# Performance work log

Hardware: AMD Instinct MI355X
Metric: run time of the kernel (lower is better)

The kernel has to match this reference:

```python
import jax, jax.numpy as jnp
import numpy as np
from jax import lax

B, E, D, N, R, K = 4, 768, 1536, 16, 48, 4
H, W = 16, 16
L = H * W
NDIR = 4


def _perms():
    idx = np.arange(L)
    idx_v = np.arange(L).reshape(H, W).T.reshape(-1)  # column-major (vertical) scan order
    perms = [idx, idx[::-1].copy(), idx_v, idx_v[::-1].copy()]
    invs = [np.argsort(p) for p in perms]
    return [jnp.asarray(p) for p in perms], [jnp.asarray(p) for p in invs]

PERMS, INVS = _perms()


def setup_inputs() -> dict:
    key = jax.random.key(0)
    ks = jax.random.split(key, 10)
    hidden_states = jax.random.normal(ks[0], (B, L, E), jnp.float32)
    in_proj_w = jax.random.normal(ks[1], (2 * D, E), jnp.float32) * 0.02
    out_proj_w = jax.random.normal(ks[2], (E, D), jnp.float32) * 0.02
    conv_w = jax.random.normal(ks[3], (NDIR, D, K), jnp.float32) * 0.1
    conv_b = jax.random.normal(ks[4], (NDIR, D), jnp.float32) * 0.1
    xproj_w = jax.random.normal(ks[5], (NDIR, R + 2 * N, D), jnp.float32) * 0.02
    dt_init_std = R ** -0.5
    dtproj_w = jax.random.uniform(ks[6], (NDIR, D, R), jnp.float32, -dt_init_std, dt_init_std)
    dt = jnp.exp(jax.random.uniform(ks[7], (NDIR, D), jnp.float32)
                 * (np.log(0.1) - np.log(0.001)) + np.log(0.001))
    dt = jnp.clip(dt, 1e-4, None)
    dtproj_b = dt + jnp.log(-jnp.expm1(-dt))  # inverse-softplus init as in the module
    A_log = jnp.broadcast_to(
        jnp.log(jnp.arange(1, N + 1, dtype=jnp.float32))[None, None, :], (NDIR, D, N)).copy()
    D_param = jnp.ones((NDIR, D), jnp.float32)
    return dict(hidden_states=hidden_states, in_proj_w=in_proj_w, out_proj_w=out_proj_w,
                conv_w=conv_w, conv_b=conv_b, xproj_w=xproj_w, dtproj_w=dtproj_w,
                dtproj_b=dtproj_b, A_log=A_log, D_param=D_param)


def _mamba_dir(xz, cw, cb, xw, dtw, dtb, a_log, dpar):
    # xz: (B, 2D, L) in this direction's scan order
    x, z = xz[:, :D], xz[:, D:]
    # causal depthwise conv1d + SiLU (mamba_inner_fn conv path)
    x = lax.conv_general_dilated(x, cw[:, None, :], (1,), [(K - 1, 0)],
                                 feature_group_count=D,
                                 dimension_numbers=('NCH', 'OIH', 'NCH'))
    x = jax.nn.silu(x + cb[None, :, None])
    # x_proj -> dt, B, C
    x_dbl = jnp.einsum('bdl,kd->bkl', x, xw)
    dt, Bm, Cm = x_dbl[:, :R], x_dbl[:, R:R + N], x_dbl[:, R + N:]
    delta = jax.nn.softplus(jnp.einsum('brl,dr->bdl', dt, dtw) + dtb[None, :, None])
    A = -jnp.exp(a_log)                                  # (D, N)
    dA = jnp.exp(jnp.einsum('bdl,dn->lbdn', delta, A))   # (L, B, D, N)
    dBu = jnp.einsum('bdl,bnl,bdl->lbdn', delta, Bm, x)  # delta * B * u

    def step(h, inp):
        da, dbu = inp
        h = da * h + dbu
        return h, h

    h0 = jnp.zeros((x.shape[0], D, N), x.dtype)
    _, hs = lax.scan(step, h0, (dA, dBu))                # (L, B, D, N)
    y = jnp.einsum('lbdn,bnl->bdl', hs, Cm) + dpar[None, :, None] * x
    return y * jax.nn.silu(z)                            # gate, (B, D, L)


def reference(hidden_states, in_proj_w, out_proj_w, conv_w, conv_b,
              xproj_w, dtproj_w, dtproj_b, A_log, D_param):
    xz = jnp.einsum('ble,fe->bfl', hidden_states, in_proj_w)  # (B, 2D, L)
    out = jnp.zeros((hidden_states.shape[0], D, L), hidden_states.dtype)
    for i in range(NDIR):  # fixed small set of structurally distinct scan directions
        xz_i = xz[:, :, PERMS[i]]
        y = _mamba_dir(xz_i, conv_w[i], conv_b[i], xproj_w[i], dtproj_w[i],
                       dtproj_b[i], A_log[i], D_param[i])
        out = out + y[:, :, INVS[i]]  # multi_reverse then sum-fusion
    return jnp.einsum('bdl,ed->ble', out, out_proj_w)
```

## Files before the change

### kernel.cpp

```cpp
#include <hip/hip_runtime.h>
#include <hip/hip_bf16.h>

#define BI   4
#define LI   256
#define EI   768
#define DI   1536
#define NI   16
#define RI   48
#define KI   4
#define NDIRS 4
#define F2D  3072
#define MROWS 1024
#define LOG2E 1.4426950408889634f
#define LN2   0.6931471805599453f

typedef float    floatx2 __attribute__((ext_vector_type(2)));
typedef float    floatx4 __attribute__((ext_vector_type(4)));
typedef _Float16 halfx2  __attribute__((ext_vector_type(2)));
typedef _Float16 halfx4  __attribute__((ext_vector_type(4)));
typedef _Float16 halfx8  __attribute__((ext_vector_type(8)));

typedef __attribute__((address_space(3))) unsigned lds_u32;
typedef __attribute__((address_space(1))) const unsigned glb_u32;

__device__ __forceinline__ void load16(const _Float16* g, _Float16* l) {
    __builtin_amdgcn_global_load_lds((glb_u32*)g, (lds_u32*)l, 16, 0, 0);
}

__device__ __forceinline__ int perm_idx(int dir, int j) {
    switch (dir) {
        case 0:  return j;
        case 1:  return 255 - j;
        case 2:  return ((j & 15) << 4) | (j >> 4);
        default: return 255 - (((j & 15) << 4) | (j >> 4));
    }
}

template<int CTRL>
__device__ __forceinline__ float dpp_add(float p) {
    int t = __builtin_amdgcn_update_dpp(0, __builtin_bit_cast(int, p),
                                        CTRL, 0xf, 0xf, true);
    return p + __builtin_bit_cast(float, t);
}
__device__ __forceinline__ float grp8_sum(float p) {
    p = dpp_add<0xB1>(p);
    p = dpp_add<0x4E>(p);
    p = dpp_add<0x141>(p);
    return p;
}

template<int BM, int BN, int WGN, int FM, int FN>
__device__ __forceinline__ void gemm_core(const _Float16* __restrict__ Ah,
                                          const _Float16* __restrict__ Al, int lda,
                                          const _Float16* __restrict__ Bh,
                                          const _Float16* __restrict__ Bl, int ldb,
                                          int nChunks, _Float16* smem,
                                          floatx4 (&acc)[FM][FN]) {
    const int tid = threadIdx.x, lane = tid & 63, wave = tid >> 6;
    const int wave_m = wave / WGN, wave_n = wave % WGN;
    _Float16* sAh = smem;
    _Float16* sAl = smem + BM * 32;
    _Float16* sBh = smem + BM * 64;
    _Float16* sBl = smem + BM * 64 + BN * 32;
    const int rr = lane & 15, koff = (lane >> 4) * 8;
    const int arow = wave_m * FM * 16, brow = wave_n * FN * 16;

    for (int c = 0; c < nChunks; ++c) {
        for (int idx = tid; idx < BM * 4; idx += 256) {
            int r = idx >> 2, s = (idx & 3) * 8;
            load16(Ah + (size_t)r * lda + c * 32 + s, sAh + idx * 8);
            load16(Al + (size_t)r * lda + c * 32 + s, sAl + idx * 8);
        }
        for (int idx = tid; idx < BN * 4; idx += 256) {
            int r = idx >> 2, s = (idx & 3) * 8;
            load16(Bh + (size_t)r * ldb + c * 32 + s, sBh + idx * 8);
            load16(Bl + (size_t)r * ldb + c * 32 + s, sBl + idx * 8);
        }
        asm volatile("s_waitcnt vmcnt(0)" ::: "memory");
        __syncthreads();

        halfx8 ahf[FM], alf[FM], bhf[FN], blf[FN];
        #pragma unroll
        for (int i = 0; i < FM; ++i) {
            ahf[i] = *(const halfx8*)(sAh + (arow + i * 16 + rr) * 32 + koff);
            alf[i] = *(const halfx8*)(sAl + (arow + i * 16 + rr) * 32 + koff);
        }
        #pragma unroll
        for (int j = 0; j < FN; ++j) {
            bhf[j] = *(const halfx8*)(sBh + (brow + j * 16 + rr) * 32 + koff);
            blf[j] = *(const halfx8*)(sBl + (brow + j * 16 + rr) * 32 + koff);
        }
        #pragma unroll
        for (int i = 0; i < FM; ++i)
            #pragma unroll
            for (int j = 0; j < FN; ++j) {
                acc[i][j] = __builtin_amdgcn_mfma_f32_16x16x32_f16(ahf[i], bhf[j], acc[i][j], 0, 0, 0);
                acc[i][j] = __builtin_amdgcn_mfma_f32_16x16x32_f16(ahf[i], blf[j], acc[i][j], 0, 0, 0);
                acc[i][j] = __builtin_amdgcn_mfma_f32_16x16x32_f16(alf[i], bhf[j], acc[i][j], 0, 0, 0);
            }
        __syncthreads();
    }
}

__global__ __launch_bounds__(256) void k_splitall(
        const float* __restrict__ hs,  const float* __restrict__ wip,
        const float* __restrict__ wop, const float* __restrict__ xw,
        const float* __restrict__ dtw,
        _Float16* __restrict__ hsh,  _Float16* __restrict__ hsl,
        _Float16* __restrict__ wiph, _Float16* __restrict__ wipl,
        _Float16* __restrict__ woph, _Float16* __restrict__ wopl,
        _Float16* __restrict__ xwh,  _Float16* __restrict__ xwl,
        _Float16* __restrict__ dtwh, _Float16* __restrict__ dtwl) {
    int i4 = (blockIdx.x * 256 + threadIdx.x) * 4;
    floatx4 v;
    _Float16 *dh, *dl; int off;
    if (i4 < 786432)        { off = i4;           v = *(const floatx4*)(hs + off);  dh = hsh;  dl = hsl;  }
    else if (i4 < 3145728)  { off = i4 - 786432;  v = *(const floatx4*)(wip + off); dh = wiph; dl = wipl; }
    else if (i4 < 4325376)  { off = i4 - 3145728; v = *(const floatx4*)(wop + off); dh = woph; dl = wopl; }
    else if (i4 < 4816896)  { off = i4 - 4325376; v = *(const floatx4*)(xw + off);  dh = xwh;  dl = xwl;  }
    else {
        int t0 = i4 - 4816896;
        int col = t0 & 63, dr = t0 >> 6;
        floatx4 z = {0.f, 0.f, 0.f, 0.f};
        v = (col < 48) ? *(const floatx4*)(dtw + (size_t)dr * 48 + col) : z;
        dh = dtwh; dl = dtwl; off = t0;
    }
    halfx4 hh, hl;
    #pragma unroll
    for (int e = 0; e < 4; ++e) {
        _Float16 h = (_Float16)v[e];
        hh[e] = h; hl[e] = (_Float16)(v[e] - (float)h);
    }
    *(halfx4*)(dh + off) = hh;
    *(halfx4*)(dl + off) = hl;
}

__global__ __launch_bounds__(256) void k_inproj_t(const _Float16* __restrict__ Ah,
                                                  const _Float16* __restrict__ Al,
                                                  const _Float16* __restrict__ Bh,
                                                  const _Float16* __restrict__ Bl,
                                                  float* __restrict__ C) {
    __shared__ _Float16 smem[128 * 64 + 128 * 64];
    int row0 = blockIdx.x * 128, col0 = blockIdx.y * 128, k0 = blockIdx.z * 384;
    float* Cp = C + (size_t)blockIdx.z * MROWS * F2D;
    floatx4 acc[4][4] = {};
    gemm_core<128, 128, 2, 4, 4>(Ah + (size_t)row0 * EI + k0, Al + (size_t)row0 * EI + k0, EI,
                                 Bh + (size_t)col0 * EI + k0, Bl + (size_t)col0 * EI + k0, EI,
                                 12, smem, acc);
    int lane = threadIdx.x & 63, wave = threadIdx.x >> 6;
    int cc = lane & 15, q = lane >> 4;
    int rbase = row0 + (wave >> 1) * 64, cbase = col0 + (wave & 1) * 64;
    #pragma unroll
    for (int i = 0; i < 4; ++i)
        #pragma unroll
        for (int j = 0; j < 4; ++j)
            #pragma unroll
            for (int r = 0; r < 4; ++r)
                Cp[(size_t)(rbase + i * 16 + q * 4 + r) * F2D + cbase + j * 16 + cc] = acc[i][j][r];
}

__global__ __launch_bounds__(256) void k_outproj_t(const _Float16* __restrict__ Ah,
                                                   const _Float16* __restrict__ Al,
                                                   const _Float16* __restrict__ Bh,
                                                   const _Float16* __restrict__ Bl,
                                                   float* __restrict__ C) {
    __shared__ _Float16 smem[192 * 64];
    int row0 = blockIdx.x * 64, col0 = blockIdx.y * 128, k0 = blockIdx.z * 384;
    float* Cp = C + (size_t)blockIdx.z * MROWS * EI;
    floatx4 acc[2][4] = {};
    gemm_core<64, 128, 2, 2, 4>(Ah + (size_t)row0 * DI + k0, Al + (size_t)row0 * DI + k0, DI,
                                Bh + (size_t)col0 * DI + k0, Bl + (size_t)col0 * DI + k0, DI,
                                12, smem, acc);
    int lane = threadIdx.x & 63, wave = threadIdx.x >> 6;
    int cc = lane & 15, q = lane >> 4;
    int rbase = row0 + (wave >> 1) * 32, cbase = col0 + (wave & 1) * 64;
    #pragma unroll
    for (int i = 0; i < 2; ++i)
        #pragma unroll
        for (int j = 0; j < 4; ++j)
            #pragma unroll
            for (int r = 0; r < 4; ++r)
                Cp[(size_t)(rbase + i * 16 + q * 4 + r) * EI + cbase + j * 16 + cc] = acc[i][j][r];
}

__global__ __launch_bounds__(256) void k_osum(const float* __restrict__ oacc,
                                              float* __restrict__ out) {
    int i4 = (blockIdx.x * 256 + threadIdx.x) * 4;
    const size_t S = (size_t)MROWS * EI;
    floatx4 s = *(const floatx4*)(oacc + i4) + *(const floatx4*)(oacc + S + i4) +
                *(const floatx4*)(oacc + 2 * S + i4) + *(const floatx4*)(oacc + 3 * S + i4);
    *(floatx4*)(out + i4) = s;
}

__global__ __launch_bounds__(256) void k_xdbl_t(const _Float16* __restrict__ xh,
                                                const _Float16* __restrict__ xl,
                                                const _Float16* __restrict__ xwh,
                                                const _Float16* __restrict__ xwl,
                                                float* __restrict__ C) {
    __shared__ _Float16 smem[208 * 64];
    int row0 = blockIdx.x * 128, dir = blockIdx.y, k0 = blockIdx.z * 192;
    float* Cp = C + (size_t)blockIdx.z * NDIRS * MROWS * 80;
    floatx4 acc[2][5] = {};
    const size_t abase = ((size_t)dir * MROWS + row0) * DI + k0;
    const size_t bbase = (size_t)dir * 80 * DI + k0;
    gemm_core<128, 80, 1, 2, 5>(xh + abase, xl + abase, DI,
                                xwh + bbase, xwl + bbase, DI, 6, smem, acc);
    int lane = threadIdx.x & 63, wave = threadIdx.x >> 6;
    int cc = lane & 15, q = lane >> 4;
    int rbase = row0 + wave * 32;
    #pragma unroll
    for (int i = 0; i < 2; ++i)
        #pragma unroll
        for (int j = 0; j < 5; ++j)
            #pragma unroll
            for (int r = 0; r < 4; ++r)
                Cp[((size_t)dir * MROWS + rbase + i * 16 + q * 4 + r) * 80 + j * 16 + cc] = acc[i][j][r];
}

__global__ __launch_bounds__(256) void k_xsplit(const float* __restrict__ acc,
                                                _Float16* __restrict__ dtqh,
                                                _Float16* __restrict__ dtql,
                                                float* __restrict__ BCm) {
    const size_t PS = (size_t)NDIRS * MROWS * 80;
    int idx = blockIdx.x * 256 + threadIdx.x;
    int dir = idx / (MROWS * 96);
    int rem = idx - dir * MROWS * 96;
    int row = rem / 96, col = rem - row * 96;
    size_t rbase = (size_t)dir * MROWS + row;
    auto sum8 = [&](int c) {
        size_t o = rbase * 80 + c;
        float s = 0.f;
        #pragma unroll
        for (int kp = 0; kp < 8; ++kp) s += acc[kp * PS + o];
        return s;
    };
    if (col < 64) {
        float v = (col < 48) ? sum8(col) : 0.f;
        _Float16 h = (_Float16)v;
        dtqh[rbase * 64 + col] = h;
        dtql[rbase * 64 + col] = (_Float16)(v - (float)h);
    } else if (col < 80) {
        int n = col - 64;
        BCm[rbase * 32 + n * 2] = sum8(48 + n);
    } else {
        int n = col - 80;
        BCm[rbase * 32 + n * 2 + 1] = sum8(64 + n);
    }
}

__global__ __launch_bounds__(512) void k_conv4(const float* __restrict__ xz,
                                               const float* __restrict__ cw,
                                               const float* __restrict__ cb,
                                               _Float16* __restrict__ xh,
                                               _Float16* __restrict__ xl) {
    const size_t S = (size_t)MROWS * F2D;
    const int b = blockIdx.y, d0 = blockIdx.x * 16;
    const int tid = threadIdx.x;
    __shared__ float sx[256][18];

    for (int i = tid; i < 1024; i += 512) {
        int row = i >> 2, c4 = (i & 3) * 4;
        size_t o = ((size_t)b * 256 + row) * F2D + d0 + c4;
        floatx4 v = *(const floatx4*)(xz + o) + *(const floatx4*)(xz + S + o);
        floatx2 v0 = {v[0], v[1]}, v1 = {v[2], v[3]};
        *(floatx2*)&sx[row][c4]     = v0;
        *(floatx2*)&sx[row][c4 + 2] = v1;
    }
    __syncthreads();

    const int dsub = tid & 15, lg = tid >> 4;
    const int d = d0 + dsub, j0 = lg * 8;
    #pragma unroll
    for (int dir = 0; dir < NDIRS; ++dir) {
        floatx4 w = *(const floatx4*)(cw + ((size_t)dir * DI + d) * KI);
        float bias = cb[(size_t)dir * DI + d];
        float xm3 = (j0 >= 3) ? sx[perm_idx(dir, j0 - 3)][dsub] : 0.f;
        float xm2 = (j0 >= 2) ? sx[perm_idx(dir, j0 - 2)][dsub] : 0.f;
        float xm1 = (j0 >= 1) ? sx[perm_idx(dir, j0 - 1)][dsub] : 0.f;
        #pragma unroll
        for (int j = 0; j < 8; ++j) {
            float cur = sx[perm_idx(dir, j0 + j)][dsub];
            float s = bias + w[0] * xm3 + w[1] * xm2 + w[2] * xm1 + w[3] * cur;
            xm3 = xm2; xm2 = xm1; xm1 = cur;
            float x = s / (1.f + __expf(-s));
            _Float16 h = (_Float16)x;
            size_t o = ((size_t)dir * MROWS + b * 256 + j0 + j) * DI + d;
            xh[o] = h;
            xl[o] = (_Float16)(x - (float)h);
        }
    }
}

__global__ __launch_bounds__(256) void k_scan(const _Float16* __restrict__ dtqh,
                                              const _Float16* __restrict__ dtql,
                                              const _Float16* __restrict__ dtwh,
                                              const _Float16* __restrict__ dtwl,
                                              const float* __restrict__ dtb,
                                              const _Float16* __restrict__ xhg,
                                              const _Float16* __restrict__ xlg,
                                              const float* __restrict__ BCm,
                                              const float* __restrict__ A_log,
                                              const float* __restrict__ Dp,
                                              float* __restrict__ ydir) {
    const int dchunk = blockIdx.x, b = blockIdx.y, dir = blockIdx.z;
    const int tid = threadIdx.x, lane = tid & 63, wave = tid >> 6;
    const int dslot = tid >> 3;
    const int np = tid & 7;
    const int d0 = dchunk * 32, d = d0 + dslot;

    __shared__ float sdx[2][32][68];
    __shared__ float sbc[2][32][32];
    __shared__ float sY[2][32][32];

    const float Av0 = -__expf(A_log[((size_t)dir * DI + d) * NI + 2 * np]) * LOG2E;
    const float Av1 = -__expf(A_log[((size_t)dir * DI + d) * NI + 2 * np + 1]) * LOG2E;
    const float Dpar = Dp[(size_t)dir * DI + d];
    float h0 = 0.f, h1 = 0.f;

    const size_t dirrow = (size_t)dir * MROWS;
    const int srow = tid >> 3, sc4 = (tid & 7) * 4;

    const int rowhalf = wave >> 1, dhalf = wave & 1;
    const int rr = lane & 15, koff = (lane >> 4) * 8, q = lane >> 4;
    const size_t bfb = ((size_t)dir * DI + d0 + dhalf * 16 + rr) * 64;
    halfx8 bhf[2], blf[2];
    bhf[0] = *(const halfx8*)(dtwh + bfb + koff);
    bhf[1] = *(const halfx8*)(dtwh + bfb + 32 + koff);
    blf[0] = *(const halfx8*)(dtwl + bfb + koff);
    blf[1] = *(const halfx8*)(dtwl + bfb + 32 + koff);
    const float bias = dtb[(size_t)dir * DI + d0 + dhalf * 16 + rr];

    floatx4 rbc;
    halfx4 rxh, rxl;
    auto load_chunk = [&](int j0) {
        int row = b * 256 + j0 + srow;
        size_t o = (dirrow + row) * DI + d0 + sc4;
        rxh = *(const halfx4*)(xhg + o);
        rxl = *(const halfx4*)(xlg + o);
        rbc = *(const floatx4*)(BCm + (dirrow + row) * 32 + sc4);
    };
    halfx8 ahf[2], alf[2];
    auto load_afrag = [&](int c) {
        size_t o = (dirrow + b * 256 + c * 32 + rowhalf * 16 + rr) * 64;
        ahf[0] = *(const halfx8*)(dtqh + o + koff);
        ahf[1] = *(const halfx8*)(dtqh + o + 32 + koff);
        alf[0] = *(const halfx8*)(dtql + o + koff);
        alf[1] = *(const halfx8*)(dtql + o + 32 + koff);
    };
    auto stage = [&](int bf) {
        #pragma unroll
        for (int e = 0; e < 4; ++e)
            sdx[bf][sc4 + e][srow * 2 + 1] = (float)rxh[e] + (float)rxl[e];
        *(floatx4*)&sbc[bf][srow][sc4] = rbc;
    };
    auto mfma_delta = [&](int bf) {
        floatx4 acc = {};
        #pragma unroll
        for (int kc = 0; kc < 2; ++kc) {
            acc = __builtin_amdgcn_mfma_f32_16x16x32_f16(ahf[kc], bhf[kc], acc, 0, 0, 0);
            acc = __builtin_amdgcn_mfma_f32_16x16x32_f16(ahf[kc], blf[kc], acc, 0, 0, 0);
            acc = __builtin_amdgcn_mfma_f32_16x16x32_f16(alf[kc], bhf[kc], acc, 0, 0, 0);
        }
        #pragma unroll
        for (int r = 0; r < 4; ++r) {
            float v = acc[r] + bias;
            float sp = (v > 20.f) ? v
                     : __log2f(1.f + __builtin_amdgcn_exp2f(v * LOG2E)) * LN2;
            sdx[bf][dhalf * 16 + rr][(rowhalf * 16 + q * 4 + r) * 2] = sp;
        }
    };

    load_chunk(0);
    load_afrag(0);
    stage(0);
    mfma_delta(0);
    load_chunk(32);
    load_afrag(1);
    __syncthreads();

    for (int c = 0; c < 8; ++c) {
        const int buf = c & 1;
        if (c < 7) {
            stage(buf ^ 1);
            mfma_delta(buf ^ 1);
            if (c < 6) { load_chunk((c + 2) * 32); load_afrag(c + 2); }
        }

        #pragma unroll
        for (int jj = 0; jj < 32; jj += 2) {
            floatx4 dxx = *(const floatx4*)&sdx[buf][dslot][jj * 2];
            #pragma unroll
            for (int t = 0; t < 2; ++t) {
                floatx4 bc = *(const floatx4*)&sbc[buf][jj + t][np * 4];
                float dv = dxx[t * 2], xv = dxx[t * 2 + 1];
                float a0 = __builtin_amdgcn_exp2f(dv * Av0);
                float a1 = __builtin_amdgcn_exp2f(dv * Av1);
                float du = dv * xv;
                h0 = fmaf(a0, h0, du * bc[0]);
                h1 = fmaf(a1, h1, du * bc[2]);
                float p = fmaf(h1, bc[3], h0 * bc[1]);
                p = grp8_sum(p);
                if (np == 0) sY[buf][jj + t][dslot] = fmaf(Dpar, xv, p);
            }
        }
        __syncthreads();

        {
            int lout = perm_idx(dir, c * 32 + srow);
            floatx4 o = *(const floatx4*)&sY[buf][srow][sc4];
            *(floatx4*)&ydir[(dirrow + (size_t)b * 256 + lout) * DI + d0 + sc4] = o;
        }
    }
}

__global__ __launch_bounds__(256) void k_sum(const float* __restrict__ ydir,
                                             const float* __restrict__ xz,
                                             _Float16* __restrict__ yh,
                                             _Float16* __restrict__ yl) {
    int i4 = (blockIdx.x * 256 + threadIdx.x) * 4;
    const size_t S = (size_t)MROWS * DI;
    const size_t SZ = (size_t)MROWS * F2D;
    int row = i4 / DI, dcol = i4 - row * DI;
    size_t zo = (size_t)row * F2D + DI + dcol;
    floatx4 zv = *(const floatx4*)(xz + zo) + *(const floatx4*)(xz + SZ + zo);
    floatx4 s = *(const floatx4*)(ydir + i4) + *(const floatx4*)(ydir + S + i4) +
                *(const floatx4*)(ydir + 2 * S + i4) + *(const floatx4*)(ydir + 3 * S + i4);
    halfx4 hh, hl;
    #pragma unroll
    for (int e = 0; e < 4; ++e) {
        float g = zv[e] / (1.f + __expf(-zv[e]));
        float v = s[e] * g;
        _Float16 h = (_Float16)v;
        hh[e] = h; hl[e] = (_Float16)(v - (float)h);
    }
    *(halfx4*)(yh + i4) = hh;
    *(halfx4*)(yl + i4) = hl;
}

extern "C" void kernel_launch(void* const* d_in, const int* in_sizes, int n_in,
                              void* d_out, int out_size, void* d_ws, size_t ws_size,
                              hipStream_t stream) {
    const float* hs   = (const float*)d_in[0];
    const float* wip  = (const float*)d_in[1];
    const float* wop  = (const float*)d_in[2];
    const float* cw   = (const float*)d_in[3];
    const float* cb   = (const float*)d_in[4];
    const float* xw   = (const float*)d_in[5];
    const float* dtw  = (const float*)d_in[6];
    const float* dtb  = (const float*)d_in[7];
    const float* alog = (const float*)d_in[8];
    const float* dpar = (const float*)d_in[9];
    float* out = (float*)d_out;

    char* p = (char*)d_ws;
    auto alloc_f32 = [&](size_t n) { float* r = (float*)p; p += n * 4; return r; };
    auto alloc_f16 = [&](size_t n) { _Float16* r = (_Float16*)p; p += n * 2; return r; };

    _Float16* hsh  = alloc_f16(786432);
    _Float16* hsl  = alloc_f16(786432);
    _Float16* wiph = alloc_f16(2359296);
    _Float16* wipl = alloc_f16(2359296);
    _Float16* woph = alloc_f16(1179648);
    _Float16* wopl = alloc_f16(1179648);
    _Float16* xwh  = alloc_f16(491520);
    _Float16* xwl  = alloc_f16(491520);
    _Float16* dtwh = alloc_f16((size_t)NDIRS * DI * 64);
    _Float16* dtwl = alloc_f16((size_t)NDIRS * DI * 64);
    float*    xz   = alloc_f32((size_t)2 * MROWS * F2D);
    _Float16* xh   = alloc_f16((size_t)NDIRS * MROWS * DI);
    _Float16* xl   = alloc_f16((size_t)NDIRS * MROWS * DI);
    _Float16* dtqh = alloc_f16((size_t)NDIRS * MROWS * 64);
    _Float16* dtql = alloc_f16((size_t)NDIRS * MROWS * 64);
    float*    BCm  = alloc_f32((size_t)NDIRS * MROWS * 32);
    float*    oacc = alloc_f32((size_t)4 * MROWS * EI);
    float*    ydir = alloc_f32((size_t)NDIRS * MROWS * DI);
    _Float16* yh   = alloc_f16((size_t)MROWS * DI);
    _Float16* yl   = alloc_f16((size_t)MROWS * DI);

    float* xdba = ydir;

    k_splitall<<<dim3(5088), 256, 0, stream>>>(hs, wip, wop, xw, dtw,
                                               hsh, hsl, wiph, wipl, woph, wopl,
                                               xwh, xwl, dtwh, dtwl);
    k_inproj_t<<<dim3(8, 24, 2), 256, 0, stream>>>(hsh, hsl, wiph, wipl, xz);
    k_conv4   <<<dim3(96, BI), 512, 0, stream>>>(xz, cw, cb, xh, xl);
    k_xdbl_t  <<<dim3(8, NDIRS, 8), 256, 0, stream>>>(xh, xl, xwh, xwl, xdba);
    k_xsplit  <<<dim3(1536), 256, 0, stream>>>(xdba, dtqh, dtql, BCm);
    k_scan    <<<dim3(DI / 32, BI, NDIRS), 256, 0, stream>>>(dtqh, dtql, dtwh, dtwl, dtb,
                                                             xh, xl, BCm, alog, dpar, ydir);
    k_sum     <<<dim3(1536), 256, 0, stream>>>(ydir, xz, yh, yl);
    k_outproj_t<<<dim3(16, 6, 4), 256, 0, stream>>>(yh, yl, woph, wopl, oacc);
    k_osum    <<<dim3(768), 256, 0, stream>>>(oacc, out);
}
```

Baseline: 210.9 us.

## Double-buffer GEMM LDS staging and shrink xdbl and scan tiles for occupancy

```diff
diff --git a/kernel.cpp b/kernel.cpp
--- a/kernel.cpp
+++ b/kernel.cpp
@@ -58,14 +58,15 @@
                                           floatx4 (&acc)[FM][FN]) {
     const int tid = threadIdx.x, lane = tid & 63, wave = tid >> 6;
     const int wave_m = wave / WGN, wave_n = wave % WGN;
-    _Float16* sAh = smem;
-    _Float16* sAl = smem + BM * 32;
-    _Float16* sBh = smem + BM * 64;
-    _Float16* sBl = smem + BM * 64 + BN * 32;
     const int rr = lane & 15, koff = (lane >> 4) * 8;
     const int arow = wave_m * FM * 16, brow = wave_n * FN * 16;
-
-    for (int c = 0; c < nChunks; ++c) {
+    constexpr int BUFSZ = (BM + BN) * 64;
+
+    auto stage = [&](int c, int bf) {
+        _Float16* sAh = smem + bf * BUFSZ;
+        _Float16* sAl = sAh + BM * 32;
+        _Float16* sBh = sAh + BM * 64;
+        _Float16* sBl = sAh + BM * 64 + BN * 32;
         for (int idx = tid; idx < BM * 4; idx += 256) {
             int r = idx >> 2, s = (idx & 3) * 8;
             load16(Ah + (size_t)r * lda + c * 32 + s, sAh + idx * 8);
@@ -76,9 +77,20 @@
             load16(Bh + (size_t)r * ldb + c * 32 + s, sBh + idx * 8);
             load16(Bl + (size_t)r * ldb + c * 32 + s, sBl + idx * 8);
         }
-        asm volatile("s_waitcnt vmcnt(0)" ::: "memory");
-        __syncthreads();
-
+    };
+
+    stage(0, 0);
+    asm volatile("s_waitcnt vmcnt(0)" ::: "memory");
+    __syncthreads();
+
+    for (int c = 0; c < nChunks; ++c) {
+        const int bf = c & 1;
+        if (c + 1 < nChunks) stage(c + 1, bf ^ 1);
+
+        const _Float16* sAh = smem + bf * BUFSZ;
+        const _Float16* sAl = sAh + BM * 32;
+        const _Float16* sBh = sAh + BM * 64;
+        const _Float16* sBl = sAh + BM * 64 + BN * 32;
         halfx8 ahf[FM], alf[FM], bhf[FN], blf[FN];
         #pragma unroll
         for (int i = 0; i < FM; ++i) {
@@ -98,6 +110,7 @@
                 acc[i][j] = __builtin_amdgcn_mfma_f32_16x16x32_f16(ahf[i], blf[j], acc[i][j], 0, 0, 0);
                 acc[i][j] = __builtin_amdgcn_mfma_f32_16x16x32_f16(alf[i], bhf[j], acc[i][j], 0, 0, 0);
             }
+        asm volatile("s_waitcnt vmcnt(0)" ::: "memory");
         __syncthreads();
     }
 }
@@ -140,7 +153,7 @@
                                                   const _Float16* __restrict__ Bh,
                                                   const _Float16* __restrict__ Bl,
                                                   float* __restrict__ C) {
-    __shared__ _Float16 smem[128 * 64 + 128 * 64];
+    __shared__ _Float16 smem[2 * 256 * 64];
     int row0 = blockIdx.x * 128, col0 = blockIdx.y * 128, k0 = blockIdx.z * 384;
     float* Cp = C + (size_t)blockIdx.z * MROWS * F2D;
     floatx4 acc[4][4] = {};
@@ -164,7 +177,7 @@
                                                    const _Float16* __restrict__ Bh,
                                                    const _Float16* __restrict__ Bl,
                                                    float* __restrict__ C) {
-    __shared__ _Float16 smem[192 * 64];
+    __shared__ _Float16 smem[2 * 192 * 64];
     int row0 = blockIdx.x * 64, col0 = blockIdx.y * 128, k0 = blockIdx.z * 384;
     float* Cp = C + (size_t)blockIdx.z * MROWS * EI;
     floatx4 acc[2][4] = {};
@@ -197,24 +210,22 @@
                                                 const _Float16* __restrict__ xwh,
                                                 const _Float16* __restrict__ xwl,
                                                 float* __restrict__ C) {
-    __shared__ _Float16 smem[208 * 64];
-    int row0 = blockIdx.x * 128, dir = blockIdx.y, k0 = blockIdx.z * 192;
+    __shared__ _Float16 smem[2 * 144 * 64];
+    int row0 = blockIdx.x * 64, dir = blockIdx.y, k0 = blockIdx.z * 192;
     float* Cp = C + (size_t)blockIdx.z * NDIRS * MROWS * 80;
-    floatx4 acc[2][5] = {};
+    floatx4 acc[1][5] = {};
     const size_t abase = ((size_t)dir * MROWS + row0) * DI + k0;
     const size_t bbase = (size_t)dir * 80 * DI + k0;
-    gemm_core<128, 80, 1, 2, 5>(xh + abase, xl + abase, DI,
-                                xwh + bbase, xwl + bbase, DI, 6, smem, acc);
+    gemm_core<64, 80, 1, 1, 5>(xh + abase, xl + abase, DI,
+                               xwh + bbase, xwl + bbase, DI, 6, smem, acc);
     int lane = threadIdx.x & 63, wave = threadIdx.x >> 6;
     int cc = lane & 15, q = lane >> 4;
-    int rbase = row0 + wave * 32;
+    int rbase = row0 + wave * 16;
     #pragma unroll
-    for (int i = 0; i < 2; ++i)
-        #pragma unroll
-        for (int j = 0; j < 5; ++j)
-            #pragma unroll
-            for (int r = 0; r < 4; ++r)
-                Cp[((size_t)dir * MROWS + rbase + i * 16 + q * 4 + r) * 80 + j * 16 + cc] = acc[i][j][r];
+    for (int j = 0; j < 5; ++j)
+        #pragma unroll
+        for (int r = 0; r < 4; ++r)
+            Cp[((size_t)dir * MROWS + rbase + q * 4 + r) * 80 + j * 16 + cc] = acc[0][j][r];
 }
 
 __global__ __launch_bounds__(256) void k_xsplit(const float* __restrict__ acc,
@@ -291,7 +302,7 @@
     }
 }
 
-__global__ __launch_bounds__(256) void k_scan(const _Float16* __restrict__ dtqh,
+__global__ __launch_bounds__(128) void k_scan(const _Float16* __restrict__ dtqh,
                                               const _Float16* __restrict__ dtql,
                                               const _Float16* __restrict__ dtwh,
                                               const _Float16* __restrict__ dtwl,
@@ -302,15 +313,16 @@
                                               const float* __restrict__ A_log,
                                               const float* __restrict__ Dp,
                                               float* __restrict__ ydir) {
-    const int dchunk = blockIdx.x, b = blockIdx.y, dir = blockIdx.z;
+    const int dchunk = (blockIdx.x & 7) * 12 + (blockIdx.x >> 3);
+    const int b = blockIdx.y, dir = blockIdx.z;
     const int tid = threadIdx.x, lane = tid & 63, wave = tid >> 6;
     const int dslot = tid >> 3;
     const int np = tid & 7;
-    const int d0 = dchunk * 32, d = d0 + dslot;
-
-    __shared__ float sdx[2][32][68];
+    const int d0 = dchunk * 16, d = d0 + dslot;
+
+    __shared__ float sdx[2][16][68];
     __shared__ float sbc[2][32][32];
-    __shared__ float sY[2][32][32];
+    __shared__ float sY[2][32][20];
 
     const float Av0 = -__expf(A_log[((size_t)dir * DI + d) * NI + 2 * np]) * LOG2E;
     const float Av1 = -__expf(A_log[((size_t)dir * DI + d) * NI + 2 * np + 1]) * LOG2E;
@@ -318,30 +330,31 @@
     float h0 = 0.f, h1 = 0.f;
 
     const size_t dirrow = (size_t)dir * MROWS;
-    const int srow = tid >> 3, sc4 = (tid & 7) * 4;
-
-    const int rowhalf = wave >> 1, dhalf = wave & 1;
+    const int srow = tid >> 2, c4 = (tid & 3) * 4, c8 = (tid & 3) * 8;
+
     const int rr = lane & 15, koff = (lane >> 4) * 8, q = lane >> 4;
-    const size_t bfb = ((size_t)dir * DI + d0 + dhalf * 16 + rr) * 64;
+    const size_t bfb = ((size_t)dir * DI + d0 + rr) * 64;
     halfx8 bhf[2], blf[2];
     bhf[0] = *(const halfx8*)(dtwh + bfb + koff);
     bhf[1] = *(const halfx8*)(dtwh + bfb + 32 + koff);
     blf[0] = *(const halfx8*)(dtwl + bfb + koff);
     blf[1] = *(const halfx8*)(dtwl + bfb + 32 + koff);
-    const float bias = dtb[(size_t)dir * DI + d0 + dhalf * 16 + rr];
-
-    floatx4 rbc;
+    const float bias = dtb[(size_t)dir * DI + d0 + rr];
+
+    floatx4 rbc0, rbc1;
     halfx4 rxh, rxl;
     auto load_chunk = [&](int j0) {
         int row = b * 256 + j0 + srow;
-        size_t o = (dirrow + row) * DI + d0 + sc4;
+        size_t o = (dirrow + row) * DI + d0 + c4;
         rxh = *(const halfx4*)(xhg + o);
         rxl = *(const halfx4*)(xlg + o);
-        rbc = *(const floatx4*)(BCm + (dirrow + row) * 32 + sc4);
+        size_t ob = (dirrow + row) * 32 + c8;
+        rbc0 = *(const floatx4*)(BCm + ob);
+        rbc1 = *(const floatx4*)(BCm + ob + 4);
     };
     halfx8 ahf[2], alf[2];
     auto load_afrag = [&](int c) {
-        size_t o = (dirrow + b * 256 + c * 32 + rowhalf * 16 + rr) * 64;
+        size_t o = (dirrow + b * 256 + c * 32 + wave * 16 + rr) * 64;
         ahf[0] = *(const halfx8*)(dtqh + o + koff);
         ahf[1] = *(const halfx8*)(dtqh + o + 32 + koff);
         alf[0] = *(const halfx8*)(dtql + o + koff);
@@ -350,8 +363,9 @@
     auto stage = [&](int bf) {
         #pragma unroll
         for (int e = 0; e < 4; ++e)
-            sdx[bf][sc4 + e][srow * 2 + 1] = (float)rxh[e] + (float)rxl[e];
-        *(floatx4*)&sbc[bf][srow][sc4] = rbc;
+            sdx[bf][c4 + e][srow * 2 + 1] = (float)rxh[e] + (float)rxl[e];
+        *(floatx4*)&sbc[bf][srow][c8]     = rbc0;
+        *(floatx4*)&sbc[bf][srow][c8 + 4] = rbc1;
     };
     auto mfma_delta = [&](int bf) {
         floatx4 acc = {};
@@ -366,7 +380,7 @@
             float v = acc[r] + bias;
             float sp = (v > 20.f) ? v
                      : __log2f(1.f + __builtin_amdgcn_exp2f(v * LOG2E)) * LN2;
-            sdx[bf][dhalf * 16 + rr][(rowhalf * 16 + q * 4 + r) * 2] = sp;
+            sdx[bf][rr][(wave * 16 + q * 4 + r) * 2] = sp;
         }
     };
 
@@ -407,8 +421,8 @@
 
         {
             int lout = perm_idx(dir, c * 32 + srow);
-            floatx4 o = *(const floatx4*)&sY[buf][srow][sc4];
-            *(floatx4*)&ydir[(dirrow + (size_t)b * 256 + lout) * DI + d0 + sc4] = o;
+            floatx4 o = *(const floatx4*)&sY[buf][srow][c4];
+            *(floatx4*)&ydir[(dirrow + (size_t)b * 256 + lout) * DI + d0 + c4] = o;
         }
     }
 }
@@ -484,10 +498,10 @@
                                                xwh, xwl, dtwh, dtwl);
     k_inproj_t<<<dim3(8, 24, 2), 256, 0, stream>>>(hsh, hsl, wiph, wipl, xz);
     k_conv4   <<<dim3(96, BI), 512, 0, stream>>>(xz, cw, cb, xh, xl);
-    k_xdbl_t  <<<dim3(8, NDIRS, 8), 256, 0, stream>>>(xh, xl, xwh, xwl, xdba);
+    k_xdbl_t  <<<dim3(16, NDIRS, 8), 256, 0, stream>>>(xh, xl, xwh, xwl, xdba);
     k_xsplit  <<<dim3(1536), 256, 0, stream>>>(xdba, dtqh, dtql, BCm);
-    k_scan    <<<dim3(DI / 32, BI, NDIRS), 256, 0, stream>>>(dtqh, dtql, dtwh, dtwl, dtb,
-                                                             xh, xl, BCm, alog, dpar, ydir);
+    k_scan    <<<dim3(96, BI, NDIRS), 128, 0, stream>>>(dtqh, dtql, dtwh, dtwl, dtb,
+                                                        xh, xl, BCm, alog, dpar, ydir);
     k_sum     <<<dim3(1536), 256, 0, stream>>>(ydir, xz, yh, yl);
     k_outproj_t<<<dim3(16, 6, 4), 256, 0, stream>>>(yh, yl, woph, wopl, oacc);
     k_osum    <<<dim3(768), 256, 0, stream>>>(oacc, out);
```

After: 209.3 us. No clear change (-0.7%).

## Double-buffer GEMM LDS staging, drop in-proj split-K, retile GEMMs, prioritize scan

Applied to the files above, without the earlier changes.

```diff
diff --git a/kernel.cpp b/kernel.cpp
--- a/kernel.cpp
+++ b/kernel.cpp
@@ -58,14 +58,15 @@
                                           floatx4 (&acc)[FM][FN]) {
     const int tid = threadIdx.x, lane = tid & 63, wave = tid >> 6;
     const int wave_m = wave / WGN, wave_n = wave % WGN;
-    _Float16* sAh = smem;
-    _Float16* sAl = smem + BM * 32;
-    _Float16* sBh = smem + BM * 64;
-    _Float16* sBl = smem + BM * 64 + BN * 32;
     const int rr = lane & 15, koff = (lane >> 4) * 8;
     const int arow = wave_m * FM * 16, brow = wave_n * FN * 16;
-
-    for (int c = 0; c < nChunks; ++c) {
+    constexpr int BUFSZ = (BM + BN) * 64;
+
+    auto stage = [&](int c, int bf) {
+        _Float16* sAh = smem + bf * BUFSZ;
+        _Float16* sAl = sAh + BM * 32;
+        _Float16* sBh = sAh + BM * 64;
+        _Float16* sBl = sAh + BM * 64 + BN * 32;
         for (int idx = tid; idx < BM * 4; idx += 256) {
             int r = idx >> 2, s = (idx & 3) * 8;
             load16(Ah + (size_t)r * lda + c * 32 + s, sAh + idx * 8);
@@ -76,9 +77,20 @@
             load16(Bh + (size_t)r * ldb + c * 32 + s, sBh + idx * 8);
             load16(Bl + (size_t)r * ldb + c * 32 + s, sBl + idx * 8);
         }
-        asm volatile("s_waitcnt vmcnt(0)" ::: "memory");
-        __syncthreads();
-
+    };
+
+    stage(0, 0);
+    asm volatile("s_waitcnt vmcnt(0)" ::: "memory");
+    __syncthreads();
+
+    for (int c = 0; c < nChunks; ++c) {
+        const int bf = c & 1;
+        if (c + 1 < nChunks) stage(c + 1, bf ^ 1);
+
+        const _Float16* sAh = smem + bf * BUFSZ;
+        const _Float16* sAl = sAh + BM * 32;
+        const _Float16* sBh = sAh + BM * 64;
+        const _Float16* sBl = sAh + BM * 64 + BN * 32;
         halfx8 ahf[FM], alf[FM], bhf[FN], blf[FN];
         #pragma unroll
         for (int i = 0; i < FM; ++i) {
@@ -98,6 +110,7 @@
                 acc[i][j] = __builtin_amdgcn_mfma_f32_16x16x32_f16(ahf[i], blf[j], acc[i][j], 0, 0, 0);
                 acc[i][j] = __builtin_amdgcn_mfma_f32_16x16x32_f16(alf[i], bhf[j], acc[i][j], 0, 0, 0);
             }
+        asm volatile("s_waitcnt vmcnt(0)" ::: "memory");
         __syncthreads();
     }
 }
@@ -140,23 +153,22 @@
                                                   const _Float16* __restrict__ Bh,
                                                   const _Float16* __restrict__ Bl,
                                                   float* __restrict__ C) {
-    __shared__ _Float16 smem[128 * 64 + 128 * 64];
-    int row0 = blockIdx.x * 128, col0 = blockIdx.y * 128, k0 = blockIdx.z * 384;
-    float* Cp = C + (size_t)blockIdx.z * MROWS * F2D;
-    floatx4 acc[4][4] = {};
-    gemm_core<128, 128, 2, 4, 4>(Ah + (size_t)row0 * EI + k0, Al + (size_t)row0 * EI + k0, EI,
-                                 Bh + (size_t)col0 * EI + k0, Bl + (size_t)col0 * EI + k0, EI,
-                                 12, smem, acc);
+    __shared__ _Float16 smem[2 * 192 * 64];
+    int row0 = blockIdx.x * 64, col0 = blockIdx.y * 128;
+    floatx4 acc[2][4] = {};
+    gemm_core<64, 128, 2, 2, 4>(Ah + (size_t)row0 * EI, Al + (size_t)row0 * EI, EI,
+                                Bh + (size_t)col0 * EI, Bl + (size_t)col0 * EI, EI,
+                                24, smem, acc);
     int lane = threadIdx.x & 63, wave = threadIdx.x >> 6;
     int cc = lane & 15, q = lane >> 4;
-    int rbase = row0 + (wave >> 1) * 64, cbase = col0 + (wave & 1) * 64;
+    int rbase = row0 + (wave >> 1) * 32, cbase = col0 + (wave & 1) * 64;
     #pragma unroll
-    for (int i = 0; i < 4; ++i)
+    for (int i = 0; i < 2; ++i)
         #pragma unroll
         for (int j = 0; j < 4; ++j)
             #pragma unroll
             for (int r = 0; r < 4; ++r)
-                Cp[(size_t)(rbase + i * 16 + q * 4 + r) * F2D + cbase + j * 16 + cc] = acc[i][j][r];
+                C[(size_t)(rbase + i * 16 + q * 4 + r) * F2D + cbase + j * 16 + cc] = acc[i][j][r];
 }
 
 __global__ __launch_bounds__(256) void k_outproj_t(const _Float16* __restrict__ Ah,
@@ -164,7 +176,7 @@
                                                    const _Float16* __restrict__ Bh,
                                                    const _Float16* __restrict__ Bl,
                                                    float* __restrict__ C) {
-    __shared__ _Float16 smem[192 * 64];
+    __shared__ _Float16 smem[2 * 192 * 64];
     int row0 = blockIdx.x * 64, col0 = blockIdx.y * 128, k0 = blockIdx.z * 384;
     float* Cp = C + (size_t)blockIdx.z * MROWS * EI;
     floatx4 acc[2][4] = {};
@@ -197,24 +209,22 @@
                                                 const _Float16* __restrict__ xwh,
                                                 const _Float16* __restrict__ xwl,
                                                 float* __restrict__ C) {
-    __shared__ _Float16 smem[208 * 64];
-    int row0 = blockIdx.x * 128, dir = blockIdx.y, k0 = blockIdx.z * 192;
+    __shared__ _Float16 smem[2 * 144 * 64];
+    int row0 = blockIdx.x * 64, dir = blockIdx.y, k0 = blockIdx.z * 192;
     float* Cp = C + (size_t)blockIdx.z * NDIRS * MROWS * 80;
-    floatx4 acc[2][5] = {};
+    floatx4 acc[1][5] = {};
     const size_t abase = ((size_t)dir * MROWS + row0) * DI + k0;
     const size_t bbase = (size_t)dir * 80 * DI + k0;
-    gemm_core<128, 80, 1, 2, 5>(xh + abase, xl + abase, DI,
-                                xwh + bbase, xwl + bbase, DI, 6, smem, acc);
+    gemm_core<64, 80, 1, 1, 5>(xh + abase, xl + abase, DI,
+                               xwh + bbase, xwl + bbase, DI, 6, smem, acc);
     int lane = threadIdx.x & 63, wave = threadIdx.x >> 6;
     int cc = lane & 15, q = lane >> 4;
-    int rbase = row0 + wave * 32;
+    int rbase = row0 + wave * 16;
     #pragma unroll
-    for (int i = 0; i < 2; ++i)
-        #pragma unroll
-        for (int j = 0; j < 5; ++j)
-            #pragma unroll
-            for (int r = 0; r < 4; ++r)
-                Cp[((size_t)dir * MROWS + rbase + i * 16 + q * 4 + r) * 80 + j * 16 + cc] = acc[i][j][r];
+    for (int j = 0; j < 5; ++j)
+        #pragma unroll
+        for (int r = 0; r < 4; ++r)
+            Cp[((size_t)dir * MROWS + rbase + q * 4 + r) * 80 + j * 16 + cc] = acc[0][j][r];
 }
 
 __global__ __launch_bounds__(256) void k_xsplit(const float* __restrict__ acc,
@@ -253,7 +263,6 @@
                                                const float* __restrict__ cb,
                                                _Float16* __restrict__ xh,
                                                _Float16* __restrict__ xl) {
-    const size_t S = (size_t)MROWS * F2D;
     const int b = blockIdx.y, d0 = blockIdx.x * 16;
     const int tid = threadIdx.x;
     __shared__ float sx[256][18];
@@ -261,7 +270,7 @@
     for (int i = tid; i < 1024; i += 512) {
         int row = i >> 2, c4 = (i & 3) * 4;
         size_t o = ((size_t)b * 256 + row) * F2D + d0 + c4;
-        floatx4 v = *(const floatx4*)(xz + o) + *(const floatx4*)(xz + S + o);
+        floatx4 v = *(const floatx4*)(xz + o);
         floatx2 v0 = {v[0], v[1]}, v1 = {v[2], v[3]};
         *(floatx2*)&sx[row][c4]     = v0;
         *(floatx2*)&sx[row][c4 + 2] = v1;
@@ -386,6 +395,7 @@
             if (c < 6) { load_chunk((c + 2) * 32); load_afrag(c + 2); }
         }
 
+        __builtin_amdgcn_s_setprio(1);
         #pragma unroll
         for (int jj = 0; jj < 32; jj += 2) {
             floatx4 dxx = *(const floatx4*)&sdx[buf][dslot][jj * 2];
@@ -403,6 +413,7 @@
                 if (np == 0) sY[buf][jj + t][dslot] = fmaf(Dpar, xv, p);
             }
         }
+        __builtin_amdgcn_s_setprio(0);
         __syncthreads();
 
         {
@@ -419,10 +430,9 @@
                                              _Float16* __restrict__ yl) {
     int i4 = (blockIdx.x * 256 + threadIdx.x) * 4;
     const size_t S = (size_t)MROWS * DI;
-    const size_t SZ = (size_t)MROWS * F2D;
     int row = i4 / DI, dcol = i4 - row * DI;
     size_t zo = (size_t)row * F2D + DI + dcol;
-    floatx4 zv = *(const floatx4*)(xz + zo) + *(const floatx4*)(xz + SZ + zo);
+    floatx4 zv = *(const floatx4*)(xz + zo);
     floatx4 s = *(const floatx4*)(ydir + i4) + *(const floatx4*)(ydir + S + i4) +
                 *(const floatx4*)(ydir + 2 * S + i4) + *(const floatx4*)(ydir + 3 * S + i4);
     halfx4 hh, hl;
@@ -466,7 +476,7 @@
     _Float16* xwl  = alloc_f16(491520);
     _Float16* dtwh = alloc_f16((size_t)NDIRS * DI * 64);
     _Float16* dtwl = alloc_f16((size_t)NDIRS * DI * 64);
-    float*    xz   = alloc_f32((size_t)2 * MROWS * F2D);
+    float*    xz   = alloc_f32((size_t)MROWS * F2D);
     _Float16* xh   = alloc_f16((size_t)NDIRS * MROWS * DI);
     _Float16* xl   = alloc_f16((size_t)NDIRS * MROWS * DI);
     _Float16* dtqh = alloc_f16((size_t)NDIRS * MROWS * 64);
@@ -482,9 +492,9 @@
     k_splitall<<<dim3(5088), 256, 0, stream>>>(hs, wip, wop, xw, dtw,
                                                hsh, hsl, wiph, wipl, woph, wopl,
                                                xwh, xwl, dtwh, dtwl);
-    k_inproj_t<<<dim3(8, 24, 2), 256, 0, stream>>>(hsh, hsl, wiph, wipl, xz);
+    k_inproj_t<<<dim3(16, 24), 256, 0, stream>>>(hsh, hsl, wiph, wipl, xz);
     k_conv4   <<<dim3(96, BI), 512, 0, stream>>>(xz, cw, cb, xh, xl);
-    k_xdbl_t  <<<dim3(8, NDIRS, 8), 256, 0, stream>>>(xh, xl, xwh, xwl, xdba);
+    k_xdbl_t  <<<dim3(16, NDIRS, 8), 256, 0, stream>>>(xh, xl, xwh, xwl, xdba);
     k_xsplit  <<<dim3(1536), 256, 0, stream>>>(xdba, dtqh, dtql, BCm);
     k_scan    <<<dim3(DI / 32, BI, NDIRS), 256, 0, stream>>>(dtqh, dtql, dtwh, dtwl, dtb,
                                                              xh, xl, BCm, alog, dpar, ydir);
```

After: 203.5 us. -3.5%, faster.
